# Optimization experiments

Hardware: AMD Instinct MI355X
Metric: run time of the kernel (lower is better)

The kernel has to match this reference:

```python
import jax, jax.numpy as jnp
import numpy as np

# arch config (matches init_kwargs)
T = 8
G = 16
D = 64
GG = G * G
THR = 0.5            # arch.object_threshold
Z_COS_MATCH_W = 5.0  # arch.z_cos_match_weight
ADJ_W = 1.0
PRES_W = 1.0
POOL_W = 1.0
OBJ_W = 10.0
FLOW_W = 1.0
FULL_OBJ = 200000.0  # arch.full_object_weight
FLOW_END = 100000.0  # arch.flow_cooling_end_step


def setup_inputs() -> dict:
    key = jax.random.key(0)
    k1, k2, k3 = jax.random.split(key, 3)
    B = 128
    return {
        "z_what": jax.random.normal(k1, (T * B, GG, D), dtype=jnp.float32),
        "z_pres_prob": jax.random.uniform(k2, (T * B, GG, 1), dtype=jnp.float32),
        "grid_flow": jax.random.uniform(k3, (T * B, GG, 1), dtype=jnp.float32),
        "global_step": 50000,
    }


def _maxpool3x3(x):
    # x: (N, C, G, G); torch MaxPool2d(3, stride=1, padding=1) pads with -inf
    return jax.lax.reduce_window(
        x, -jnp.inf, jax.lax.max,
        window_dimensions=(1, 1, 3, 3), window_strides=(1, 1, 1, 1),
        padding=[(0, 0), (0, 0), (1, 1), (1, 1)])


def reference(z_what, z_pres_prob, grid_flow, global_step):
    B = z_what.shape[0] // T
    zw = z_what.reshape(T, B, GG, D)
    zp = z_pres_prob.reshape(T, B, GG, 1)

    # ---- z_what_loss_grid_cell: adjacent squared deltas ----
    z_what_loss = jnp.sum((zw[1:] - zw[:-1]) ** 2)

    # ---- z_pres_loss_grid_cell ----
    sim = 1.0 - (zp[2:] - zp[:-2]) ** 2
    deltas = (zp[2:] - zp[1:-1]) ** 2 + (zp[:-2] - zp[1:-1]) ** 2
    z_pres_loss = jnp.sum(sim * deltas)

    # ---- z_what_consistency_pool (cosine_sim branch) ----
    w = jnp.abs(zw) * zp                                    # (T,B,GG,D)
    wi = w.transpose(0, 1, 3, 2).reshape(T * B, D, G, G)
    smoothed = _maxpool3x3(wi).reshape(T, B, D, GG).transpose(0, 1, 3, 2)
    dot = jnp.sum(smoothed[:-1] * w[1:], axis=-1)           # (T-1,B,GG)
    na = jnp.maximum(jnp.sqrt(jnp.sum(smoothed[:-1] ** 2, -1)), 1e-6)
    nb = jnp.maximum(jnp.sqrt(jnp.sum(w[1:] ** 2, -1)), 1e-6)
    cos_pool = dot / (na * nb)
    pw = zp[..., 0]
    pw = (pw[:-1] + pw[1:]) * 0.5                           # (T-1,B,GG)
    z_what_loss_pool = -jnp.sum(cos_pool * pw)

    # ---- z_what_consistency_objects (vectorized over objects) ----
    # For every active cell (t,b,i,j) at time t<T-1, compare its z_what (prior)
    # with z_what at t+1 over the 3x3 circular neighborhood, restricted to
    # neighbor cells whose z_pres > threshold. Loss per object:
    #   -z_cos_match_weight * max(sim) + sum(sim); skipped if no active neighbor.
    zpg = zp.reshape(T, B, G, G)
    zwg = zw.reshape(T, B, G, G, D)
    prior = zwg[:-1]                                        # (T-1,B,G,G,D)
    prior_n = jnp.maximum(jnp.sqrt(jnp.sum(prior ** 2, -1)), 1e-8)
    pres_prior = zpg[:-1] > THR                             # (T-1,B,G,G)
    sum_sim = jnp.zeros(prior.shape[:-1], dtype=prior.dtype)
    max_sim = jnp.full(prior.shape[:-1], -jnp.inf, dtype=prior.dtype)
    has_nb = jnp.zeros(prior.shape[:-1], dtype=bool)
    for di in (-1, 0, 1):
        for dj in (-1, 0, 1):
            nbw = jnp.roll(zwg[1:], (-di, -dj), axis=(2, 3))       # circular
            nbp = jnp.roll(zpg[1:], (-di, -dj), axis=(2, 3)) > THR
            dotn = jnp.sum(prior * nbw, axis=-1)
            nn = jnp.maximum(jnp.sqrt(jnp.sum(nbw ** 2, -1)), 1e-8)
            s = dotn / (prior_n * nn)
            sum_sim = sum_sim + jnp.where(nbp, s, 0.0)
            max_sim = jnp.maximum(max_sim, jnp.where(nbp, s, -jnp.inf))
            has_nb = has_nb | nbp
    valid = pres_prior & has_nb
    contrib = jnp.where(valid, -Z_COS_MATCH_W * max_sim + sum_sim, 0.0)
    z_what_loss_objects = jnp.sum(contrib)
    objects_detected = jnp.sum(pres_prior.astype(jnp.int32))

    # ---- compute_flow_loss ----
    zp_img = z_pres_prob.reshape(-1, 1, G, G)
    zp_max = _maxpool3x3(zp_img).reshape(-1, GG, 1)
    flow = grid_flow.reshape(-1, GG, 1)
    fmask = flow > 0.5
    flow_loss = jnp.sum(jnp.where(fmask, (zp_max - flow) ** 2, 0.0)) \
        + 100.0 * jnp.maximum(0.0, jnp.sum(zp_img) - jnp.sum(flow))

    # ---- total (Space base loss excluded; external submodule) ----
    scale_obj = min(1.0, float(global_step) / FULL_OBJ)
    scale_flow = max(0.0, 1.0 - float(global_step) / FLOW_END)
    loss = (z_what_loss * ADJ_W
            + z_pres_loss * PRES_W
            + z_what_loss_pool * POOL_W
            + z_what_loss_objects * scale_obj * OBJ_W
            + flow_loss * FLOW_W * scale_flow)
    return loss
```

## Files before the change

### kernel.cpp

```cpp
#include <hip/hip_runtime.h>
#include <math.h>

#define TT 8
#define BB 128
#define GG 256
#define DD 64
#define NCH 4
#define CF4 4
#define ST 5


__device__ inline float wred(float v) {
#pragma unroll
    for (int off = 32; off > 0; off >>= 1) v += __shfl_xor(v, off, 64);
    return v;
}
__device__ inline float dot4(float4 a, float4 b) {
    return a.x * b.x + a.y * b.y + a.z * b.z + a.w * b.w;
}
__device__ inline float4 fabs4(float4 a) {
    return make_float4(fabsf(a.x), fabsf(a.y), fabsf(a.z), fabsf(a.w));
}
__device__ inline float4 max4(float4 a, float4 b) {
    return make_float4(fmaxf(a.x, b.x), fmaxf(a.y, b.y), fmaxf(a.z, b.z), fmaxf(a.w, b.w));
}
__device__ inline float4 scale4(float4 a, float s) {
    return make_float4(a.x * s, a.y * s, a.z * s, a.w * s);
}
__device__ inline float4 sub4(float4 a, float4 b) {
    return make_float4(a.x - b.x, a.y - b.y, a.z - b.z, a.w - b.w);
}

__global__ __launch_bounds__(256) void pair_kernel(const float* __restrict__ zw,
                                                   const float* __restrict__ zp,
                                                   const float* __restrict__ flow,
                                                   float* __restrict__ ws) {
    const int pairIdx = blockIdx.x;
    const int t = pairIdx >> 7;
    const int b = pairIdx & (BB - 1);
    const int tid = threadIdx.x;
    const int gi = tid >> 4, gj = tid & 15;

    __shared__ float4 shW[GG * ST];
    __shared__ float4 shB[GG * ST];
    __shared__ float pA[GG], pB[GG], nB[GG];
    __shared__ float bred[8][4];

    const float4* gA = (const float4*)zw + (size_t)(t * BB + b) * 1024;
    const float4* gB = gA + (size_t)BB * 1024;

    const float pAc = zp[(size_t)(t * BB + b) * GG + tid];
    const float pBc = zp[(size_t)((t + 1) * BB + b) * GG + tid];
    pA[tid] = pAc;
    pB[tid] = pBc;

    int nbc[9];
    unsigned inbM = 0;
    {
        int m = 0;
#pragma unroll
        for (int di = -1; di <= 1; di++) {
#pragma unroll
            for (int dj = -1; dj <= 1; dj++) {
                nbc[m] = (((gi + di) & 15) << 4) | ((gj + dj) & 15);
                if (((unsigned)(gi + di) < 16u) && ((unsigned)(gj + dj) < 16u))
                    inbM |= (1u << m);
                m++;
            }
        }
    }
    __syncthreads();

    float zdiff = 0.f, sa = 0.f, sb = 0.f, poolDot = 0.f, poolN = 0.f;
    float dots[9] = {0.f, 0.f, 0.f, 0.f, 0.f, 0.f, 0.f, 0.f, 0.f};

#pragma unroll 1
    for (int c = 0; c < NCH; c++) {
        float4 aA[CF4], aB[CF4];
#pragma unroll
        for (int q = 0; q < CF4; q++) {
            aA[q] = gA[tid * 16 + c * 4 + q];
            aB[q] = gB[tid * 16 + c * 4 + q];
        }
#pragma unroll
        for (int q = 0; q < CF4; q++) {
            float4 d = sub4(aB[q], aA[q]);
            zdiff += dot4(d, d);
            sa += dot4(aA[q], aA[q]);
            sb += dot4(aB[q], aB[q]);
            dots[4] += dot4(aA[q], aB[q]);
            shW[tid * ST + q] = scale4(fabs4(aA[q]), pAc);
            shB[tid * ST + q] = aB[q];
        }
        __syncthreads();

#pragma unroll
        for (int k = 0; k < 9; k++) {
            if (k == 4) continue;
            int base = nbc[k] * ST;
#pragma unroll
            for (int q = 0; q < CF4; q++) dots[k] += dot4(aA[q], shB[base + q]);
        }

        float4 rm[CF4];
#pragma unroll
        for (int q = 0; q < CF4; q++) rm[q] = scale4(fabs4(aA[q]), pAc);
        if (gj > 0) {
            int base = (tid - 1) * ST;
#pragma unroll
            for (int q = 0; q < CF4; q++) rm[q] = max4(rm[q], shW[base + q]);
        }
        if (gj < 15) {
            int base = (tid + 1) * ST;
#pragma unroll
            for (int q = 0; q < CF4; q++) rm[q] = max4(rm[q], shW[base + q]);
        }
        __syncthreads();
#pragma unroll
        for (int q = 0; q < CF4; q++) shB[tid * ST + q] = rm[q];
        __syncthreads();

        float4 sm[CF4];
#pragma unroll
        for (int q = 0; q < CF4; q++) sm[q] = rm[q];
        if (gi > 0) {
            int base = (tid - 16) * ST;
#pragma unroll
            for (int q = 0; q < CF4; q++) sm[q] = max4(sm[q], shB[base + q]);
        }
        if (gi < 15) {
            int base = (tid + 16) * ST;
#pragma unroll
            for (int q = 0; q < CF4; q++) sm[q] = max4(sm[q], shB[base + q]);
        }
#pragma unroll
        for (int q = 0; q < CF4; q++) {
            poolDot += dot4(sm[q], fabs4(aB[q]));
            poolN += dot4(sm[q], sm[q]);
        }
        __syncthreads();
    }

    nB[tid] = sqrtf(sb);
    __syncthreads();

    float prior_n = fmaxf(sqrtf(sa), 1e-8f);
    float sum_sim = 0.f, max_sim = -1e30f;
    bool has = false;
#pragma unroll
    for (int k = 0; k < 9; k++) {
        float nn = fmaxf(nB[nbc[k]], 1e-8f);
        float s = dots[k] / (prior_n * nn);
        if (pB[nbc[k]] > 0.5f) {
            sum_sim += s;
            max_sim = fmaxf(max_sim, s);
            has = true;
        }
    }
    float obj = ((pAc > 0.5f) && has) ? (sum_sim - 5.0f * max_sim) : 0.f;

    float na_pool = fmaxf(sqrtf(poolN), 1e-6f);
    float nb_pool = fmaxf(pBc * sqrtf(sb), 1e-6f);
    float poolc = -(pBc * poolDot) / (na_pool * nb_pool) * 0.5f * (pAc + pBc);

    float mx = pAc;
#pragma unroll
    for (int k = 0; k < 9; k++)
        if (k != 4 && ((inbM >> k) & 1u)) mx = fmaxf(mx, pA[nbc[k]]);
    float f = flow[(size_t)(t * BB + b) * GG + tid];
    float fsq = 0.f;
    if (f > 0.5f) { float d = mx - f; fsq = d * d; }
    float szp = pAc, sflow = f;
    if (t == 6) {
        float mxB = pBc;
#pragma unroll
        for (int k = 0; k < 9; k++)
            if (k != 4 && ((inbM >> k) & 1u)) mxB = fmaxf(mxB, pB[nbc[k]]);
        float f7 = flow[(size_t)(7 * BB + b) * GG + tid];
        if (f7 > 0.5f) { float d = mxB - f7; fsq += d * d; }
        szp += pBc;
        sflow += f7;
    }

    float pres = 0.f;
    if (t <= 5) {
        float pC = zp[(size_t)((t + 2) * BB + b) * GG + tid];
        float s02 = pC - pAc;
        float sim = 1.f - s02 * s02;
        float d2 = pC - pBc, d0 = pAc - pBc;
        pres = sim * (d2 * d2 + d0 * d0);
    }

    float r[7] = {zdiff, pres, poolc, obj, fsq, szp, sflow};
    int w = tid >> 6, lane = tid & 63;
#pragma unroll
    for (int j = 0; j < 7; j++) {
        float rv = wred(r[j]);
        if (lane == 0) bred[j][w] = rv;
    }
    __syncthreads();
    if (tid < 7)
        ws[pairIdx * 8 + tid] = bred[tid][0] + bred[tid][1] + bred[tid][2] + bred[tid][3];
}

__global__ __launch_bounds__(256) void final_kernel(const float* __restrict__ ws,
                                                    const int* __restrict__ gs,
                                                    float* __restrict__ out) {
    const int tid = threadIdx.x;
    __shared__ float bred[7][4];
    float c[7] = {0.f, 0.f, 0.f, 0.f, 0.f, 0.f, 0.f};
    for (int p = tid; p < (TT - 1) * BB; p += 256) {
        const float* r = ws + p * 8;
#pragma unroll
        for (int j = 0; j < 7; j++) c[j] += r[j];
    }
    int w = tid >> 6, lane = tid & 63;
#pragma unroll
    for (int j = 0; j < 7; j++) {
        float rv = wred(c[j]);
        if (lane == 0) bred[j][w] = rv;
    }
    __syncthreads();
    if (tid == 0) {
        float s[7];
#pragma unroll
        for (int j = 0; j < 7; j++) s[j] = bred[j][0] + bred[j][1] + bred[j][2] + bred[j][3];
        float step = (float)gs[0];
        float scale_obj = fminf(1.f, step / 200000.f);
        float scale_flow = fmaxf(0.f, 1.f - step / 100000.f);
        float flow_loss = s[4] + 100.f * fmaxf(0.f, s[5] - s[6]);
        out[0] = s[0]
               + s[1]
               + s[2]
               + s[3] * scale_obj * 10.0f
               + flow_loss * scale_flow;
    }
}

extern "C" void kernel_launch(void* const* d_in, const int* in_sizes, int n_in,
                              void* d_out, int out_size, void* d_ws, size_t ws_size,
                              hipStream_t stream) {
    const float* zw = (const float*)d_in[0];
    const float* zp = (const float*)d_in[1];
    const float* fl = (const float*)d_in[2];
    const int* gs = (const int*)d_in[3];
    float* ws = (float*)d_ws;

    pair_kernel<<<(TT - 1) * BB, 256, 0, stream>>>(zw, zp, fl, ws);
    final_kernel<<<1, 256, 0, stream>>>(ws, gs, (float*)d_out);
}
```

Measured before the change: 130.2 us.

## Use DPP row max for pooling, drop shW LDS, fuse final reduction

Result: slower. 253.8 us (+94.9%).

```diff
diff --git a/kernel.cpp b/kernel.cpp
--- a/kernel.cpp
+++ b/kernel.cpp
@@ -31,20 +31,31 @@
     return make_float4(a.x - b.x, a.y - b.y, a.z - b.z, a.w - b.w);
 }
 
-__global__ __launch_bounds__(256) void pair_kernel(const float* __restrict__ zw,
-                                                   const float* __restrict__ zp,
-                                                   const float* __restrict__ flow,
-                                                   float* __restrict__ ws) {
+__device__ inline float rowmax3(float v) {
+    int iv = __float_as_int(v);
+    int a = __builtin_amdgcn_update_dpp(iv, iv, 0x101, 0xF, 0xF, false);
+    int c = __builtin_amdgcn_update_dpp(iv, iv, 0x111, 0xF, 0xF, false);
+    return fmaxf(v, fmaxf(__int_as_float(a), __int_as_float(c)));
+}
+__device__ inline float4 rowmax3_4(float4 v) {
+    return make_float4(rowmax3(v.x), rowmax3(v.y), rowmax3(v.z), rowmax3(v.w));
+}
+
+__global__ __launch_bounds__(256, 4) void pair_kernel(const float* __restrict__ zw,
+                                                      const float* __restrict__ zp,
+                                                      const float* __restrict__ flow,
+                                                      const int* __restrict__ gs,
+                                                      float* __restrict__ ws,
+                                                      float* __restrict__ out) {
     const int pairIdx = blockIdx.x;
     const int t = pairIdx >> 7;
     const int b = pairIdx & (BB - 1);
     const int tid = threadIdx.x;
     const int gi = tid >> 4, gj = tid & 15;
 
-    __shared__ float4 shW[GG * ST];
     __shared__ float4 shB[GG * ST];
     __shared__ float pA[GG], pB[GG], nB[GG];
-    __shared__ float bred[8][4];
+    __shared__ float bred[7][4];
 
     const float4* gA = (const float4*)zw + (size_t)(t * BB + b) * 1024;
     const float4* gB = gA + (size_t)BB * 1024;
@@ -73,6 +84,7 @@
 
     float zdiff = 0.f, sa = 0.f, sb = 0.f, poolDot = 0.f, poolN = 0.f;
     float dots[9] = {0.f, 0.f, 0.f, 0.f, 0.f, 0.f, 0.f, 0.f, 0.f};
+    const int sbase = tid * ST;
 
 #pragma unroll 1
     for (int c = 0; c < NCH; c++) {
@@ -82,6 +94,15 @@
             aA[q] = gA[tid * 16 + c * 4 + q];
             aB[q] = gB[tid * 16 + c * 4 + q];
         }
+
+        float4 rm[CF4];
+#pragma unroll
+        for (int q = 0; q < CF4; q++) {
+            shB[sbase + q] = aB[q];
+            rm[q] = rowmax3_4(scale4(fabs4(aA[q]), pAc));
+        }
+        __syncthreads();
+
 #pragma unroll
         for (int q = 0; q < CF4; q++) {
             float4 d = sub4(aB[q], aA[q]);
@@ -89,11 +110,7 @@
             sa += dot4(aA[q], aA[q]);
             sb += dot4(aB[q], aB[q]);
             dots[4] += dot4(aA[q], aB[q]);
-            shW[tid * ST + q] = scale4(fabs4(aA[q]), pAc);
-            shB[tid * ST + q] = aB[q];
-        }
-        __syncthreads();
-
+        }
 #pragma unroll
         for (int k = 0; k < 9; k++) {
             if (k == 4) continue;
@@ -101,23 +118,10 @@
 #pragma unroll
             for (int q = 0; q < CF4; q++) dots[k] += dot4(aA[q], shB[base + q]);
         }
-
-        float4 rm[CF4];
-#pragma unroll
-        for (int q = 0; q < CF4; q++) rm[q] = scale4(fabs4(aA[q]), pAc);
-        if (gj > 0) {
-            int base = (tid - 1) * ST;
-#pragma unroll
-            for (int q = 0; q < CF4; q++) rm[q] = max4(rm[q], shW[base + q]);
-        }
-        if (gj < 15) {
-            int base = (tid + 1) * ST;
-#pragma unroll
-            for (int q = 0; q < CF4; q++) rm[q] = max4(rm[q], shW[base + q]);
-        }
-        __syncthreads();
-#pragma unroll
-        for (int q = 0; q < CF4; q++) shB[tid * ST + q] = rm[q];
+        __syncthreads();
+
+#pragma unroll
+        for (int q = 0; q < CF4; q++) shB[sbase + q] = rm[q];
         __syncthreads();
 
         float4 sm[CF4];
@@ -199,41 +203,30 @@
         if (lane == 0) bred[j][w] = rv;
     }
     __syncthreads();
-    if (tid < 7)
-        ws[pairIdx * 8 + tid] = bred[tid][0] + bred[tid][1] + bred[tid][2] + bred[tid][3];
-}
-
-__global__ __launch_bounds__(256) void final_kernel(const float* __restrict__ ws,
-                                                    const int* __restrict__ gs,
-                                                    float* __restrict__ out) {
-    const int tid = threadIdx.x;
-    __shared__ float bred[7][4];
-    float c[7] = {0.f, 0.f, 0.f, 0.f, 0.f, 0.f, 0.f};
-    for (int p = tid; p < (TT - 1) * BB; p += 256) {
-        const float* r = ws + p * 8;
-#pragma unroll
-        for (int j = 0; j < 7; j++) c[j] += r[j];
-    }
-    int w = tid >> 6, lane = tid & 63;
-#pragma unroll
-    for (int j = 0; j < 7; j++) {
-        float rv = wred(c[j]);
-        if (lane == 0) bred[j][w] = rv;
-    }
-    __syncthreads();
+    if (tid < 7) {
+        float v = bred[tid][0] + bred[tid][1] + bred[tid][2] + bred[tid][3];
+        atomicAdd(&ws[tid], v);
+    }
+    __syncthreads();
+
     if (tid == 0) {
-        float s[7];
-#pragma unroll
-        for (int j = 0; j < 7; j++) s[j] = bred[j][0] + bred[j][1] + bred[j][2] + bred[j][3];
-        float step = (float)gs[0];
-        float scale_obj = fminf(1.f, step / 200000.f);
-        float scale_flow = fmaxf(0.f, 1.f - step / 100000.f);
-        float flow_loss = s[4] + 100.f * fmaxf(0.f, s[5] - s[6]);
-        out[0] = s[0]
-               + s[1]
-               + s[2]
-               + s[3] * scale_obj * 10.0f
-               + flow_loss * scale_flow;
+        unsigned old = __hip_atomic_fetch_add((unsigned*)(ws + 7), 1u,
+                                              __ATOMIC_ACQ_REL, __HIP_MEMORY_SCOPE_AGENT);
+        if (old == (unsigned)(gridDim.x - 1)) {
+            float s[7];
+#pragma unroll
+            for (int j = 0; j < 7; j++)
+                s[j] = __hip_atomic_load(ws + j, __ATOMIC_RELAXED, __HIP_MEMORY_SCOPE_AGENT);
+            float step = (float)gs[0];
+            float scale_obj = fminf(1.f, step / 200000.f);
+            float scale_flow = fmaxf(0.f, 1.f - step / 100000.f);
+            float flow_loss = s[4] + 100.f * fmaxf(0.f, s[5] - s[6]);
+            out[0] = s[0]
+                   + s[1]
+                   + s[2]
+                   + s[3] * scale_obj * 10.0f
+                   + flow_loss * scale_flow;
+        }
     }
 }
 
@@ -246,6 +239,6 @@
     const int* gs = (const int*)d_in[3];
     float* ws = (float*)d_ws;
 
-    pair_kernel<<<(TT - 1) * BB, 256, 0, stream>>>(zw, zp, fl, ws);
-    final_kernel<<<1, 256, 0, stream>>>(ws, gs, (float*)d_out);
-}
+    hipMemsetAsync(d_ws, 0, 8 * sizeof(float), stream);
+    pair_kernel<<<(TT - 1) * BB, 256, 0, stream>>>(zw, zp, fl, gs, ws, (float*)d_out);
+}
```

## Use DPP row max for horizontal pooling and prefetch next chunk into registers

Applied to the files above, without the earlier changes.

Result: slower. 141.4 us (+8.6%).

```diff
diff --git a/kernel.cpp b/kernel.cpp
--- a/kernel.cpp
+++ b/kernel.cpp
@@ -29,6 +29,16 @@
 }
 __device__ inline float4 sub4(float4 a, float4 b) {
     return make_float4(a.x - b.x, a.y - b.y, a.z - b.z, a.w - b.w);
+}
+
+__device__ inline float rowmax3(float v) {
+    int iv = __float_as_int(v);
+    int a = __builtin_amdgcn_update_dpp(iv, iv, 0x101, 0xF, 0xF, false);
+    int c = __builtin_amdgcn_update_dpp(iv, iv, 0x111, 0xF, 0xF, false);
+    return fmaxf(v, fmaxf(__int_as_float(a), __int_as_float(c)));
+}
+__device__ inline float4 rowmax3_4(float4 v) {
+    return make_float4(rowmax3(v.x), rowmax3(v.y), rowmax3(v.z), rowmax3(v.w));
 }
 
 __global__ __launch_bounds__(256) void pair_kernel(const float* __restrict__ zw,
@@ -41,10 +51,10 @@
     const int tid = threadIdx.x;
     const int gi = tid >> 4, gj = tid & 15;
 
-    __shared__ float4 shW[GG * ST];
     __shared__ float4 shB[GG * ST];
-    __shared__ float pA[GG], pB[GG], nB[GG];
-    __shared__ float bred[8][4];
+    __shared__ float4 shM[GG * ST];
+    __shared__ float pA[GG], pB[GG], nrmB[GG];
+    __shared__ float bred[7][4];
 
     const float4* gA = (const float4*)zw + (size_t)(t * BB + b) * 1024;
     const float4* gB = gA + (size_t)BB * 1024;
@@ -69,19 +79,37 @@
             }
         }
     }
-    __syncthreads();
 
     float zdiff = 0.f, sa = 0.f, sb = 0.f, poolDot = 0.f, poolN = 0.f;
     float dots[9] = {0.f, 0.f, 0.f, 0.f, 0.f, 0.f, 0.f, 0.f, 0.f};
+    const int sbase = tid * ST;
+
+    float4 aA[CF4], aB[CF4];
+#pragma unroll
+    for (int q = 0; q < CF4; q++) {
+        aA[q] = gA[tid * 16 + q];
+        aB[q] = gB[tid * 16 + q];
+    }
 
 #pragma unroll 1
     for (int c = 0; c < NCH; c++) {
-        float4 aA[CF4], aB[CF4];
-#pragma unroll
-        for (int q = 0; q < CF4; q++) {
-            aA[q] = gA[tid * 16 + c * 4 + q];
-            aB[q] = gB[tid * 16 + c * 4 + q];
-        }
+        float4 pfA[CF4], pfB[CF4];
+        const int cn = (c + 1) & 3;
+#pragma unroll
+        for (int q = 0; q < CF4; q++) {
+            pfA[q] = gA[tid * 16 + cn * 4 + q];
+            pfB[q] = gB[tid * 16 + cn * 4 + q];
+        }
+
+        float4 rm[CF4];
+#pragma unroll
+        for (int q = 0; q < CF4; q++) {
+            shB[sbase + q] = aB[q];
+            rm[q] = rowmax3_4(scale4(fabs4(aA[q]), pAc));
+            shM[sbase + q] = rm[q];
+        }
+        __syncthreads();
+
 #pragma unroll
         for (int q = 0; q < CF4; q++) {
             float4 d = sub4(aB[q], aA[q]);
@@ -89,11 +117,7 @@
             sa += dot4(aA[q], aA[q]);
             sb += dot4(aB[q], aB[q]);
             dots[4] += dot4(aA[q], aB[q]);
-            shW[tid * ST + q] = scale4(fabs4(aA[q]), pAc);
-            shB[tid * ST + q] = aB[q];
-        }
-        __syncthreads();
-
+        }
 #pragma unroll
         for (int k = 0; k < 9; k++) {
             if (k == 4) continue;
@@ -101,47 +125,28 @@
 #pragma unroll
             for (int q = 0; q < CF4; q++) dots[k] += dot4(aA[q], shB[base + q]);
         }
-
-        float4 rm[CF4];
-#pragma unroll
-        for (int q = 0; q < CF4; q++) rm[q] = scale4(fabs4(aA[q]), pAc);
-        if (gj > 0) {
-            int base = (tid - 1) * ST;
-#pragma unroll
-            for (int q = 0; q < CF4; q++) rm[q] = max4(rm[q], shW[base + q]);
-        }
-        if (gj < 15) {
-            int base = (tid + 1) * ST;
-#pragma unroll
-            for (int q = 0; q < CF4; q++) rm[q] = max4(rm[q], shW[base + q]);
-        }
-        __syncthreads();
-#pragma unroll
-        for (int q = 0; q < CF4; q++) shB[tid * ST + q] = rm[q];
-        __syncthreads();
-
-        float4 sm[CF4];
-#pragma unroll
-        for (int q = 0; q < CF4; q++) sm[q] = rm[q];
         if (gi > 0) {
             int base = (tid - 16) * ST;
 #pragma unroll
-            for (int q = 0; q < CF4; q++) sm[q] = max4(sm[q], shB[base + q]);
+            for (int q = 0; q < CF4; q++) rm[q] = max4(rm[q], shM[base + q]);
         }
         if (gi < 15) {
             int base = (tid + 16) * ST;
 #pragma unroll
-            for (int q = 0; q < CF4; q++) sm[q] = max4(sm[q], shB[base + q]);
-        }
-#pragma unroll
-        for (int q = 0; q < CF4; q++) {
-            poolDot += dot4(sm[q], fabs4(aB[q]));
-            poolN += dot4(sm[q], sm[q]);
+            for (int q = 0; q < CF4; q++) rm[q] = max4(rm[q], shM[base + q]);
+        }
+#pragma unroll
+        for (int q = 0; q < CF4; q++) {
+            poolDot += dot4(rm[q], fabs4(aB[q]));
+            poolN += dot4(rm[q], rm[q]);
         }
         __syncthreads();
-    }
-
-    nB[tid] = sqrtf(sb);
+
+#pragma unroll
+        for (int q = 0; q < CF4; q++) { aA[q] = pfA[q]; aB[q] = pfB[q]; }
+    }
+
+    nrmB[tid] = sqrtf(sb);
     __syncthreads();
 
     float prior_n = fmaxf(sqrtf(sa), 1e-8f);
@@ -149,7 +154,7 @@
     bool has = false;
 #pragma unroll
     for (int k = 0; k < 9; k++) {
-        float nn = fmaxf(nB[nbc[k]], 1e-8f);
+        float nn = fmaxf(nrmB[nbc[k]], 1e-8f);
         float s = dots[k] / (prior_n * nn);
         if (pB[nbc[k]] > 0.5f) {
             sum_sim += s;
```
